# Optimization experiments

Measured on AMD Instinct MI355X. Metric: run time of the kernel, lower is better.

## Reference

```python
import jax, jax.numpy as jnp
import numpy as np

B, T, V = 4, 2048, 2048
D, H, L = 512, 8, 4
HD = D // H


def setup_inputs() -> dict:
    key = jax.random.key(0)
    ks = jax.random.split(key, 8)
    inp = {
        "x": jax.random.normal(ks[0], (B, T, V), dtype=jnp.float32),
        "token_embedding": jax.random.normal(ks[1], (D, V), dtype=jnp.float32),
        "position_embedding": jax.random.normal(ks[2], (T, D), dtype=jnp.float32),
        "Wk": jax.random.normal(ks[3], (L, D, D), dtype=jnp.float32),
        "Wq": jax.random.normal(ks[4], (L, D, D), dtype=jnp.float32),
        "Wv": jax.random.normal(ks[5], (L, D, D), dtype=jnp.float32),
        "Wp": jax.random.normal(ks[6], (L, D, D), dtype=jnp.float32),
        "readout": jax.random.normal(ks[7], (V, D), dtype=jnp.float32),
    }
    return inp


def _attention_block(h, wk, wq, wv, wp):
    # h: [B, T, D]; weights [D, D] (inner_dim == D since head_dim*num_heads == D)
    b, t, c = h.shape
    s = c ** (-0.5)

    def proj(w):
        # F.linear(h, w) = h @ w.T -> [B,T,D] -> [B,H,T,HD], scaled by C^{-1/2}
        return (jnp.einsum('btc,dc->btd', h, w) * s).reshape(b, t, H, HD).transpose(0, 2, 1, 3)

    q, k, v = proj(wq), proj(wk), proj(wv)
    scores = jnp.einsum('bhqd,bhkd->bhqk', q, k) * (HD ** (-0.5))  # [B,H,T,T]
    attn = jax.nn.softmax(scores, axis=-1)
    out = jnp.einsum('bhqk,bhkd->bhqd', attn, v)  # [B,H,T,HD]
    out = out.transpose(0, 2, 1, 3).reshape(b, t, c)
    # projection.size(-1) == inner_dim == D
    return jnp.einsum('btc,oc->bto', out, wp) * (c ** (-0.5))


def reference(x, token_embedding, position_embedding, Wk, Wq, Wv, Wp, readout):
    b, t, c = x.shape  # c == vocab_size
    tok = jnp.einsum('btv,dv->btd', x, token_embedding) * (c ** (-0.5))
    h = tok + position_embedding[:t]
    for l in range(L):
        h = _attention_block(h, Wk[l], Wq[l], Wv[l], Wp[l])
    # logits on last token; readout.size(-1) == D
    logits = jnp.einsum('bd,vd->bv', h[:, -1, :], readout) * (D ** (-0.5))
    return logits
```

## Files before the change

### kernel.cpp

```cpp
#include <hip/hip_runtime.h>
#include <math.h>

typedef __attribute__((ext_vector_type(4))) float    f32x4;
typedef __attribute__((ext_vector_type(2))) _Float16 f16x2;
typedef __attribute__((ext_vector_type(4))) _Float16 f16x4;
typedef __attribute__((ext_vector_type(8))) _Float16 f16x8;

constexpr int Bc  = 4;
constexpr int Tc  = 2048;
constexpr int Vc  = 2048;
constexpr int Dc  = 512;
constexpr int Hc  = 8;
constexpr int HDc = 64;
constexpr int Lc  = 4;
constexpr size_t SZe = (size_t)Bc * Tc * Dc;

constexpr float SM_C = 12.0f;

__device__ __forceinline__ void gload_lds16(const _Float16* g, _Float16* s) {
    __builtin_amdgcn_global_load_lds(
        (const __attribute__((address_space(1))) void*)g,
        (__attribute__((address_space(3))) void*)s,
        16, 0, 0);
}

__device__ __forceinline__ f16x2 cvt_pk(float a, float b) {
    return __builtin_bit_cast(f16x2, __builtin_amdgcn_cvt_pkrtz(a, b));
}

__global__ __launch_bounds__(256) void cvt_k(
    const float* __restrict__ in, _Float16* __restrict__ out, int n4)
{
    for (int i = blockIdx.x * 256 + threadIdx.x; i < n4; i += gridDim.x * 256) {
        float4 v = ((const float4*)in)[i];
        f16x4 h = {(_Float16)v.x, (_Float16)v.y, (_Float16)v.z, (_Float16)v.w};
        *(f16x4*)&out[(size_t)i * 4] = h;
    }
}

__global__ __launch_bounds__(256) void cvtW_k(
    const float* __restrict__ a, const float* __restrict__ b,
    const float* __restrict__ c, const float* __restrict__ d,
    _Float16* __restrict__ oa, _Float16* __restrict__ ob,
    _Float16* __restrict__ oc, _Float16* __restrict__ od, int n4)
{
    const float* in; _Float16* out;
    switch (blockIdx.y) {
        case 0:  in = a; out = oa; break;
        case 1:  in = b; out = ob; break;
        case 2:  in = c; out = oc; break;
        default: in = d; out = od; break;
    }
    for (int i = blockIdx.x * 256 + threadIdx.x; i < n4; i += gridDim.x * 256) {
        float4 v = ((const float4*)in)[i];
        f16x4 h = {(_Float16)v.x, (_Float16)v.y, (_Float16)v.z, (_Float16)v.w};
        *(f16x4*)&out[(size_t)i * 4] = h;
    }
}


template<bool QKV>
__global__ __launch_bounds__(256) void gemm_f16(
    const _Float16* __restrict__ A,
    const _Float16* __restrict__ W0, const _Float16* __restrict__ W1,
    const _Float16* __restrict__ W2,
    void* __restrict__ C0, const float* __restrict__ pos,
    int K, float scA, float scB)
{
    __shared__ __align__(16) _Float16 LA[2][128 * 64];
    __shared__ __align__(16) _Float16 LB[2][64 * 64];

    const int tid = threadIdx.x;
    const int w  = tid >> 6, l = tid & 63;
    const int li = l & 15,  lg = l >> 4;
    const int wm = w >> 1,  wn = w & 1;
    const int m0 = blockIdx.x * 128;

    int sec = 0, n0;
    const _Float16* Wb;
    if (QKV) {
        sec = blockIdx.y >> 3; n0 = (blockIdx.y & 7) * 64;
        Wb = (sec == 0) ? W0 : ((sec == 1) ? W1 : W2);
    } else {
        n0 = blockIdx.y * 64; Wb = W0;
    }
    const float scale = (sec == 0) ? scA : scB;

    const _Float16* srcA[4];
    const _Float16* srcB[2];
#pragma unroll
    for (int i = 0; i < 4; ++i) {
        const int d = i * 4096 + tid * 16;
        const int r = d >> 7, cb = (d & 127) ^ ((r & 7) << 4);
        srcA[i] = A + (size_t)(m0 + r) * K + (cb >> 1);
    }
#pragma unroll
    for (int i = 0; i < 2; ++i) {
        const int d = i * 4096 + tid * 16;
        const int r = d >> 7, cb = (d & 127) ^ ((r & 7) << 4);
        srcB[i] = Wb + (size_t)(n0 + r) * K + (cb >> 1);
    }

    auto stage = [&](int b) {
#pragma unroll
        for (int i = 0; i < 4; ++i) { gload_lds16(srcA[i], &LA[b][i * 2048 + tid * 8]); srcA[i] += 64; }
#pragma unroll
        for (int i = 0; i < 2; ++i) { gload_lds16(srcB[i], &LB[b][i * 2048 + tid * 8]); srcB[i] += 64; }
    };

    f32x4 acc[4][2];
#pragma unroll
    for (int i = 0; i < 4; ++i)
#pragma unroll
        for (int j = 0; j < 2; ++j) acc[i][j] = (f32x4){0.f, 0.f, 0.f, 0.f};

    auto compute = [&](int b) {
        const char* Ab = (const char*)&LA[b][0];
        const char* Bb = (const char*)&LB[b][0];
        f16x8 af[4][2], bf[2][2];
#pragma unroll
        for (int mb = 0; mb < 4; ++mb) {
            const int row = wm * 64 + mb * 16 + li, sz = (row & 7) << 4;
#pragma unroll
            for (int fi = 0; fi < 2; ++fi)
                af[mb][fi] = *(const f16x8*)(Ab + row * 128 + ((fi * 64 + lg * 16) ^ sz));
        }
#pragma unroll
        for (int nb = 0; nb < 2; ++nb) {
            const int row = wn * 32 + nb * 16 + li, sz = (row & 7) << 4;
#pragma unroll
            for (int fi = 0; fi < 2; ++fi)
                bf[nb][fi] = *(const f16x8*)(Bb + row * 128 + ((fi * 64 + lg * 16) ^ sz));
        }
#pragma unroll
        for (int mb = 0; mb < 4; ++mb)
#pragma unroll
            for (int nb = 0; nb < 2; ++nb)
#pragma unroll
                for (int fi = 0; fi < 2; ++fi)
                    acc[mb][nb] = __builtin_amdgcn_mfma_f32_16x16x32_f16(
                        af[mb][fi], bf[nb][fi], acc[mb][nb], 0, 0, 0);
    };

    const int NTk = K >> 6;
    stage(0);
    for (int kt = 0; kt < NTk; ++kt) {
        const int cur = kt & 1;
        if (kt + 1 < NTk) {
            stage(cur ^ 1);
            asm volatile("s_waitcnt vmcnt(6)" ::: "memory");
        } else {
            asm volatile("s_waitcnt vmcnt(0)" ::: "memory");
        }
        __builtin_amdgcn_s_barrier();
        __builtin_amdgcn_sched_barrier(0);
        compute(cur);
        __builtin_amdgcn_s_barrier();
        __builtin_amdgcn_sched_barrier(0);
    }

#pragma unroll
    for (int mb = 0; mb < 4; ++mb) {
#pragma unroll
        for (int nb = 0; nb < 2; ++nb) {
            const int mbase = m0 + wm * 64 + mb * 16 + lg * 4;
            const int nc    = n0 + wn * 32 + nb * 16 + li;
            if (QKV && sec == 2) {
                const int t = mbase & (Tc - 1);
                const int bh2 = (mbase >> 11) * Hc + (nc >> 6), d = nc & 63;
                f16x4 vv;
#pragma unroll
                for (int r = 0; r < 4; ++r) vv[r] = (_Float16)(acc[mb][nb][r] * scale);
                _Float16* vf = (_Float16*)C0 + 2 * SZe;
                const size_t adr =
                    (((size_t)bh2 * 32 + (t >> 6)) * 8 + ((d >> 4) & 3) * 2 + ((t >> 5) & 1)) * 512
                    + ((d & 15) + 16 * ((t >> 2) & 3)) * 8 + ((t >> 4) & 1) * 4;
                *(f16x4*)&vf[adr] = vv;
            } else if (QKV && sec == 1) {
                _Float16* kf = (_Float16*)C0 + SZe;
                const int t0 = mbase & (Tc - 1);
                const int bh2 = (mbase >> 11) * Hc + (nc >> 6), d = nc & 63;
                const size_t adr0 =
                    (((size_t)bh2 * 32 + (t0 >> 6)) * 8 + ((t0 >> 4) & 3) * 2 + (d >> 5)) * 512
                    + ((t0 & 15) + 16 * ((d >> 3) & 3)) * 8 + (d & 7);
#pragma unroll
                for (int r = 0; r < 4; ++r)
                    kf[adr0 + (size_t)r * 8] = (_Float16)(acc[mb][nb][r] * scale);
            } else if (QKV) {
                _Float16* outp = (_Float16*)C0;
#pragma unroll
                for (int r = 0; r < 4; ++r) {
                    const int m = mbase + r, bb2 = m >> 11, t = m & (Tc - 1);
                    outp[(((size_t)bb2 * Hc + (nc >> 6)) * Tc + t) * HDc + (nc & 63)] =
                        (_Float16)(acc[mb][nb][r] * scale);
                }
            } else {
                _Float16* outp = (_Float16*)C0;
#pragma unroll
                for (int r = 0; r < 4; ++r) {
                    const int m = mbase + r;
                    float val = acc[mb][nb][r] * scale;
                    if (pos) val += pos[(size_t)(m & (Tc - 1)) * Dc + nc];
                    outp[(size_t)m * Dc + nc] = (_Float16)val;
                }
            }
        }
    }
}

__global__ __launch_bounds__(256) void attn_mfma(
    const _Float16* __restrict__ Qh, const _Float16* __restrict__ Kf,
    const _Float16* __restrict__ Vf, _Float16* __restrict__ o)
{
    __shared__ __align__(16) _Float16 Ks[2][4096];
    __shared__ __align__(16) _Float16 Vs[2][4096];

    const int bid = blockIdx.x;
    const int bh  = bid & 31;
    const int qt  = bid >> 5;
    const int hh  = bh & (Hc - 1);
    const int bb  = bh >> 3;
    const int tid = threadIdx.x;
    const int w   = tid >> 6;
    const int l   = tid & 63;
    const int li  = l & 15, lg = l >> 4;
    const int q0  = qt * 64 + w * 16;

    const _Float16* Qb = Qh + (size_t)bh * Tc * HDc;

    f16x8 qf[2];
#pragma unroll
    for (int fi = 0; fi < 2; ++fi)
        qf[fi] = *(const f16x8*)&Qb[(size_t)(q0 + li) * HDc + fi * 32 + lg * 8];

    const _Float16* sK0 = Kf + (size_t)bh * Tc * HDc + tid * 8;
    const _Float16* sK1 = sK0 + 2048;
    const _Float16* sV0 = Vf + (size_t)bh * Tc * HDc + tid * 8;
    const _Float16* sV1 = sV0 + 2048;

    auto stage = [&](int b) {
        gload_lds16(sK0, &Ks[b][tid * 8]);
        gload_lds16(sK1, &Ks[b][2048 + tid * 8]);
        gload_lds16(sV0, &Vs[b][tid * 8]);
        gload_lds16(sV1, &Vs[b][2048 + tid * 8]);
        sK0 += 4096; sK1 += 4096; sV0 += 4096; sV1 += 4096;
    };

    f32x4 oacc[4];
#pragma unroll
    for (int dt = 0; dt < 4; ++dt) oacc[dt] = (f32x4){0.f, 0.f, 0.f, 0.f};
    f32x4 lacc = (f32x4){0.f, 0.f, 0.f, 0.f};
    const f16x4 ones = (f16x4){(_Float16)1.f, (_Float16)1.f, (_Float16)1.f, (_Float16)1.f};

    stage(0);
    constexpr int NT = Tc / 64;
    for (int kt = 0; kt < NT; ++kt) {
        const int cur = kt & 1;
        if (kt + 1 < NT) {
            stage(cur ^ 1);
            asm volatile("s_waitcnt vmcnt(4)" ::: "memory");
        } else {
            asm volatile("s_waitcnt vmcnt(0)" ::: "memory");
        }
        __builtin_amdgcn_s_barrier();
        __builtin_amdgcn_sched_barrier(0);

        const _Float16* KL = &Ks[cur][0];
        const _Float16* VL = &Vs[cur][0];

        f32x4 s[4];
        __builtin_amdgcn_s_setprio(1);
#pragma unroll
        for (int t = 0; t < 4; ++t) {
            s[t] = (f32x4){-SM_C, -SM_C, -SM_C, -SM_C};
#pragma unroll
            for (int fi = 0; fi < 2; ++fi) {
                f16x8 kfr = *(const f16x8*)(KL + (t * 2 + fi) * 512 + l * 8);
                s[t] = __builtin_amdgcn_mfma_f32_16x16x32_f16(kfr, qf[fi], s[t], 0, 0, 0);
            }
        }
        __builtin_amdgcn_s_setprio(0);

        f16x4 pf[4];
#pragma unroll
        for (int t = 0; t < 4; ++t) {
            float p0 = __builtin_amdgcn_exp2f(s[t][0]);
            float p1 = __builtin_amdgcn_exp2f(s[t][1]);
            float p2 = __builtin_amdgcn_exp2f(s[t][2]);
            float p3 = __builtin_amdgcn_exp2f(s[t][3]);
            f16x2 lo = cvt_pk(p0, p1);
            f16x2 hi = cvt_pk(p2, p3);
            pf[t] = (f16x4){lo[0], lo[1], hi[0], hi[1]};
        }

        __builtin_amdgcn_s_setprio(1);
#pragma unroll
        for (int t = 0; t < 4; ++t)
            lacc = __builtin_amdgcn_mfma_f32_16x16x16f16(ones, pf[t], lacc, 0, 0, 0);
#pragma unroll
        for (int dt = 0; dt < 4; ++dt) {
#pragma unroll
            for (int m = 0; m < 2; ++m) {
                f16x8 vv = *(const f16x8*)(VL + (dt * 2 + m) * 512 + l * 8);
                f16x4 vlo = (f16x4){vv[0], vv[1], vv[2], vv[3]};
                f16x4 vhi = (f16x4){vv[4], vv[5], vv[6], vv[7]};
                oacc[dt] = __builtin_amdgcn_mfma_f32_16x16x16f16(vlo, pf[2 * m],     oacc[dt], 0, 0, 0);
                oacc[dt] = __builtin_amdgcn_mfma_f32_16x16x16f16(vhi, pf[2 * m + 1], oacc[dt], 0, 0, 0);
            }
        }
        __builtin_amdgcn_s_setprio(0);

        __builtin_amdgcn_s_barrier();
        __builtin_amdgcn_sched_barrier(0);
    }

    const float inv = 1.f / lacc[0];
    _Float16* op = o + ((size_t)(bb * Tc + q0 + li) * Dc + hh * HDc + lg * 4);
#pragma unroll
    for (int dt = 0; dt < 4; ++dt) {
        f16x4 rv = {(_Float16)(oacc[dt][0] * inv), (_Float16)(oacc[dt][1] * inv),
                    (_Float16)(oacc[dt][2] * inv), (_Float16)(oacc[dt][3] * inv)};
        *(f16x4*)(op + dt * 16) = rv;
    }
}

__global__ __launch_bounds__(256) void readout_k(
    const _Float16* __restrict__ h, const float* __restrict__ ro,
    float* __restrict__ out, float scale)
{
    const int idx = blockIdx.x * 256 + threadIdx.x;
    const int vv  = idx & (Vc - 1);
    const int bb  = idx >> 11;
    const _Float16* hp = h + (size_t)(bb * Tc + (Tc - 1)) * Dc;
    const float* rp = ro + (size_t)vv * Dc;
    float ax = 0.f, ay = 0.f, az = 0.f, aw = 0.f;
#pragma unroll 8
    for (int i = 0; i < Dc / 4; ++i) {
        f16x4  hv = *(const f16x4*)(hp + i * 4);
        float4 rv = *(const float4*)(rp + i * 4);
        ax = fmaf((float)hv[0], rv.x, ax);
        ay = fmaf((float)hv[1], rv.y, ay);
        az = fmaf((float)hv[2], rv.z, az);
        aw = fmaf((float)hv[3], rv.w, aw);
    }
    out[idx] = ((ax + ay) + (az + aw)) * scale;
}

extern "C" void kernel_launch(void* const* d_in, const int* in_sizes, int n_in,
                              void* d_out, int out_size, void* d_ws, size_t ws_size,
                              hipStream_t stream)
{
    const float* x    = (const float*)d_in[0];
    const float* temb = (const float*)d_in[1];
    const float* pemb = (const float*)d_in[2];
    const float* Wk   = (const float*)d_in[3];
    const float* Wq   = (const float*)d_in[4];
    const float* Wv   = (const float*)d_in[5];
    const float* Wp   = (const float*)d_in[6];
    const float* ro   = (const float*)d_in[7];
    float* out = (float*)d_out;

    _Float16* h16    = (_Float16*)d_ws;
    _Float16* temb16 = h16 + SZe;
    _Float16* wq16   = temb16 + (size_t)Dc * Vc;
    _Float16* wk16   = wq16 + (size_t)Lc * Dc * Dc;
    _Float16* wv16   = wk16 + (size_t)Lc * Dc * Dc;
    _Float16* wp16   = wv16 + (size_t)Lc * Dc * Dc;
    _Float16* o16    = wp16 + (size_t)Lc * Dc * Dc;
    _Float16* qh     = o16 + SZe;
    _Float16* khF    = qh + SZe;
    _Float16* vhF    = khF + SZe;
    _Float16* x16    = o16;

    const float s_emb  = 1.0f / sqrtf((float)Vc);
    const float s_proj = 1.0f / sqrtf((float)Dc);
    const float s_q    = s_proj * 0.125f * 1.44269504f;

    const int W4 = Lc * Dc * Dc / 4;
    cvt_k<<<2048, 256, 0, stream>>>(x, x16, (int)SZe);
    cvt_k<<<512, 256, 0, stream>>>(temb, temb16, Dc * Vc / 4);
    cvtW_k<<<dim3(512, 4), 256, 0, stream>>>(Wq, Wk, Wv, Wp,
                                             wq16, wk16, wv16, wp16, W4);

    gemm_f16<false><<<dim3(64, 8), 256, 0, stream>>>(
        x16, temb16, nullptr, nullptr, h16, pemb, Vc, s_emb, s_emb);

    const size_t WOFF = (size_t)Dc * Dc;
    for (int lyr = 0; lyr < Lc; ++lyr) {
        gemm_f16<true><<<dim3(64, 24), 256, 0, stream>>>(
            h16, wq16 + lyr * WOFF, wk16 + lyr * WOFF, wv16 + lyr * WOFF,
            qh, nullptr, Dc, s_q, s_proj);

        attn_mfma<<<Bc * Hc * (Tc / 64), 256, 0, stream>>>(qh, khF, vhF, o16);

        gemm_f16<false><<<dim3(64, 8), 256, 0, stream>>>(
            o16, wp16 + lyr * WOFF, nullptr, nullptr, h16, nullptr, Dc, s_proj, s_proj);
    }

    readout_k<<<(Bc * Vc) / 256, 256, 0, stream>>>(h16, ro, out, s_proj);
}
```

Baseline: 409.9 us.

## Switch attention to 32x32x16 MFMA with two-wave blocks and permlane32 P transpose

```diff
diff --git a/kernel.cpp b/kernel.cpp
--- a/kernel.cpp
+++ b/kernel.cpp
@@ -1,10 +1,12 @@
 #include <hip/hip_runtime.h>
 #include <math.h>
 
-typedef __attribute__((ext_vector_type(4))) float    f32x4;
-typedef __attribute__((ext_vector_type(2))) _Float16 f16x2;
-typedef __attribute__((ext_vector_type(4))) _Float16 f16x4;
-typedef __attribute__((ext_vector_type(8))) _Float16 f16x8;
+typedef __attribute__((ext_vector_type(4)))  float    f32x4;
+typedef __attribute__((ext_vector_type(16))) float    f32x16;
+typedef __attribute__((ext_vector_type(2)))  _Float16 f16x2;
+typedef __attribute__((ext_vector_type(4)))  _Float16 f16x4;
+typedef __attribute__((ext_vector_type(8)))  _Float16 f16x8;
+typedef __attribute__((ext_vector_type(4)))  unsigned u32x4;
 
 constexpr int Bc  = 4;
 constexpr int Tc  = 2048;
@@ -24,8 +26,8 @@
         16, 0, 0);
 }
 
-__device__ __forceinline__ f16x2 cvt_pk(float a, float b) {
-    return __builtin_bit_cast(f16x2, __builtin_amdgcn_cvt_pkrtz(a, b));
+__device__ __forceinline__ unsigned cvt_pk_u(float a, float b) {
+    return __builtin_bit_cast(unsigned, __builtin_amdgcn_cvt_pkrtz(a, b));
 }
 
 __global__ __launch_bounds__(256) void cvt_k(
@@ -166,23 +168,23 @@
             const int mbase = m0 + wm * 64 + mb * 16 + lg * 4;
             const int nc    = n0 + wn * 32 + nb * 16 + li;
             if (QKV && sec == 2) {
-                const int t = mbase & (Tc - 1);
+                const int t0 = mbase & (Tc - 1);
                 const int bh2 = (mbase >> 11) * Hc + (nc >> 6), d = nc & 63;
                 f16x4 vv;
 #pragma unroll
                 for (int r = 0; r < 4; ++r) vv[r] = (_Float16)(acc[mb][nb][r] * scale);
                 _Float16* vf = (_Float16*)C0 + 2 * SZe;
                 const size_t adr =
-                    (((size_t)bh2 * 32 + (t >> 6)) * 8 + ((d >> 4) & 3) * 2 + ((t >> 5) & 1)) * 512
-                    + ((d & 15) + 16 * ((t >> 2) & 3)) * 8 + ((t >> 4) & 1) * 4;
+                    (((size_t)bh2 * 32 + (t0 >> 6)) * 8 + (d >> 5) * 4 + ((t0 >> 4) & 3)) * 512
+                    + ((d & 31) + 32 * ((t0 >> 3) & 1)) * 8 + (t0 & 7);
                 *(f16x4*)&vf[adr] = vv;
             } else if (QKV && sec == 1) {
                 _Float16* kf = (_Float16*)C0 + SZe;
                 const int t0 = mbase & (Tc - 1);
                 const int bh2 = (mbase >> 11) * Hc + (nc >> 6), d = nc & 63;
                 const size_t adr0 =
-                    (((size_t)bh2 * 32 + (t0 >> 6)) * 8 + ((t0 >> 4) & 3) * 2 + (d >> 5)) * 512
-                    + ((t0 & 15) + 16 * ((d >> 3) & 3)) * 8 + (d & 7);
+                    (((size_t)bh2 * 32 + (t0 >> 6)) * 8 + ((t0 >> 5) & 1) * 4 + (d >> 4)) * 512
+                    + ((t0 & 31) + 32 * ((d >> 3) & 1)) * 8 + (d & 7);
 #pragma unroll
                 for (int r = 0; r < 4; ++r)
                     kf[adr0 + (size_t)r * 8] = (_Float16)(acc[mb][nb][r] * scale);
@@ -208,7 +210,7 @@
     }
 }
 
-__global__ __launch_bounds__(256) void attn_mfma(
+__global__ __launch_bounds__(128) void attn_mfma(
     const _Float16* __restrict__ Qh, const _Float16* __restrict__ Kf,
     const _Float16* __restrict__ Vf, _Float16* __restrict__ o)
 {
@@ -223,34 +225,31 @@
     const int tid = threadIdx.x;
     const int w   = tid >> 6;
     const int l   = tid & 63;
-    const int li  = l & 15, lg = l >> 4;
-    const int q0  = qt * 64 + w * 16;
+    const int li  = l & 31, lg = l >> 5;
+    const int q0  = qt * 64 + w * 32;
 
     const _Float16* Qb = Qh + (size_t)bh * Tc * HDc;
-
-    f16x8 qf[2];
-#pragma unroll
-    for (int fi = 0; fi < 2; ++fi)
-        qf[fi] = *(const f16x8*)&Qb[(size_t)(q0 + li) * HDc + fi * 32 + lg * 8];
-
-    const _Float16* sK0 = Kf + (size_t)bh * Tc * HDc + tid * 8;
-    const _Float16* sK1 = sK0 + 2048;
-    const _Float16* sV0 = Vf + (size_t)bh * Tc * HDc + tid * 8;
-    const _Float16* sV1 = sV0 + 2048;
-
+    f16x8 qf[4];
+#pragma unroll
+    for (int fi = 0; fi < 4; ++fi)
+        qf[fi] = *(const f16x8*)&Qb[(size_t)(q0 + li) * HDc + fi * 16 + lg * 8];
+
+    const _Float16* sK = Kf + (size_t)bh * Tc * HDc + tid * 8;
+    const _Float16* sV = Vf + (size_t)bh * Tc * HDc + tid * 8;
     auto stage = [&](int b) {
-        gload_lds16(sK0, &Ks[b][tid * 8]);
-        gload_lds16(sK1, &Ks[b][2048 + tid * 8]);
-        gload_lds16(sV0, &Vs[b][tid * 8]);
-        gload_lds16(sV1, &Vs[b][2048 + tid * 8]);
-        sK0 += 4096; sK1 += 4096; sV0 += 4096; sV1 += 4096;
+#pragma unroll
+        for (int i = 0; i < 4; ++i) gload_lds16(sK + i * 1024, &Ks[b][i * 1024 + tid * 8]);
+#pragma unroll
+        for (int i = 0; i < 4; ++i) gload_lds16(sV + i * 1024, &Vs[b][i * 1024 + tid * 8]);
+        sK += 4096; sV += 4096;
     };
 
-    f32x4 oacc[4];
-#pragma unroll
-    for (int dt = 0; dt < 4; ++dt) oacc[dt] = (f32x4){0.f, 0.f, 0.f, 0.f};
-    f32x4 lacc = (f32x4){0.f, 0.f, 0.f, 0.f};
-    const f16x4 ones = (f16x4){(_Float16)1.f, (_Float16)1.f, (_Float16)1.f, (_Float16)1.f};
+    f32x16 oacc0, oacc1, lacc, sinit;
+#pragma unroll
+    for (int i = 0; i < 16; ++i) { oacc0[i] = 0.f; oacc1[i] = 0.f; lacc[i] = 0.f; sinit[i] = -SM_C; }
+    f16x8 ones;
+#pragma unroll
+    for (int i = 0; i < 8; ++i) ones[i] = (_Float16)1.f;
 
     stage(0);
     constexpr int NT = Tc / 64;
@@ -258,7 +257,7 @@
         const int cur = kt & 1;
         if (kt + 1 < NT) {
             stage(cur ^ 1);
-            asm volatile("s_waitcnt vmcnt(4)" ::: "memory");
+            asm volatile("s_waitcnt vmcnt(8)" ::: "memory");
         } else {
             asm volatile("s_waitcnt vmcnt(0)" ::: "memory");
         }
@@ -268,45 +267,52 @@
         const _Float16* KL = &Ks[cur][0];
         const _Float16* VL = &Vs[cur][0];
 
-        f32x4 s[4];
         __builtin_amdgcn_s_setprio(1);
-#pragma unroll
-        for (int t = 0; t < 4; ++t) {
-            s[t] = (f32x4){-SM_C, -SM_C, -SM_C, -SM_C};
-#pragma unroll
-            for (int fi = 0; fi < 2; ++fi) {
-                f16x8 kfr = *(const f16x8*)(KL + (t * 2 + fi) * 512 + l * 8);
-                s[t] = __builtin_amdgcn_mfma_f32_16x16x32_f16(kfr, qf[fi], s[t], 0, 0, 0);
-            }
+        f16x8 k00 = *(const f16x8*)(KL + 0 * 512 + l * 8);
+        f16x8 k10 = *(const f16x8*)(KL + 4 * 512 + l * 8);
+        f32x16 s0 = __builtin_amdgcn_mfma_f32_32x32x16_f16(k00, qf[0], sinit, 0, 0, 0);
+        f32x16 s1 = __builtin_amdgcn_mfma_f32_32x32x16_f16(k10, qf[0], sinit, 0, 0, 0);
+#pragma unroll
+        for (int fi = 1; fi < 4; ++fi) {
+            f16x8 ka = *(const f16x8*)(KL + (0 + fi) * 512 + l * 8);
+            f16x8 kb = *(const f16x8*)(KL + (4 + fi) * 512 + l * 8);
+            s0 = __builtin_amdgcn_mfma_f32_32x32x16_f16(ka, qf[fi], s0, 0, 0, 0);
+            s1 = __builtin_amdgcn_mfma_f32_32x32x16_f16(kb, qf[fi], s1, 0, 0, 0);
         }
         __builtin_amdgcn_s_setprio(0);
 
-        f16x4 pf[4];
-#pragma unroll
-        for (int t = 0; t < 4; ++t) {
-            float p0 = __builtin_amdgcn_exp2f(s[t][0]);
-            float p1 = __builtin_amdgcn_exp2f(s[t][1]);
-            float p2 = __builtin_amdgcn_exp2f(s[t][2]);
-            float p3 = __builtin_amdgcn_exp2f(s[t][3]);
-            f16x2 lo = cvt_pk(p0, p1);
-            f16x2 hi = cvt_pk(p2, p3);
-            pf[t] = (f16x4){lo[0], lo[1], hi[0], hi[1]};
+        unsigned cc[16];
+#pragma unroll
+        for (int g = 0; g < 4; ++g) {
+            cc[2 * g]     = cvt_pk_u(__builtin_amdgcn_exp2f(s0[4 * g + 0]),
+                                     __builtin_amdgcn_exp2f(s0[4 * g + 1]));
+            cc[2 * g + 1] = cvt_pk_u(__builtin_amdgcn_exp2f(s0[4 * g + 2]),
+                                     __builtin_amdgcn_exp2f(s0[4 * g + 3]));
+            cc[8 + 2 * g]     = cvt_pk_u(__builtin_amdgcn_exp2f(s1[4 * g + 0]),
+                                         __builtin_amdgcn_exp2f(s1[4 * g + 1]));
+            cc[8 + 2 * g + 1] = cvt_pk_u(__builtin_amdgcn_exp2f(s1[4 * g + 2]),
+                                         __builtin_amdgcn_exp2f(s1[4 * g + 3]));
+        }
+
+        f16x8 Bf[4];
+#pragma unroll
+        for (int ks = 0; ks < 4; ++ks) {
+            auto u = __builtin_amdgcn_permlane32_swap(cc[ks * 4 + 0], cc[ks * 4 + 2], false, false);
+            auto v = __builtin_amdgcn_permlane32_swap(cc[ks * 4 + 1], cc[ks * 4 + 3], false, false);
+            u32x4 b4 = (u32x4){u[0], v[0], u[1], v[1]};
+            Bf[ks] = __builtin_bit_cast(f16x8, b4);
         }
 
         __builtin_amdgcn_s_setprio(1);
 #pragma unroll
-        for (int t = 0; t < 4; ++t)
-            lacc = __builtin_amdgcn_mfma_f32_16x16x16f16(ones, pf[t], lacc, 0, 0, 0);
-#pragma unroll
-        for (int dt = 0; dt < 4; ++dt) {
-#pragma unroll
-            for (int m = 0; m < 2; ++m) {
-                f16x8 vv = *(const f16x8*)(VL + (dt * 2 + m) * 512 + l * 8);
-                f16x4 vlo = (f16x4){vv[0], vv[1], vv[2], vv[3]};
-                f16x4 vhi = (f16x4){vv[4], vv[5], vv[6], vv[7]};
-                oacc[dt] = __builtin_amdgcn_mfma_f32_16x16x16f16(vlo, pf[2 * m],     oacc[dt], 0, 0, 0);
-                oacc[dt] = __builtin_amdgcn_mfma_f32_16x16x16f16(vhi, pf[2 * m + 1], oacc[dt], 0, 0, 0);
-            }
+        for (int ks = 0; ks < 4; ++ks)
+            lacc = __builtin_amdgcn_mfma_f32_32x32x16_f16(ones, Bf[ks], lacc, 0, 0, 0);
+#pragma unroll
+        for (int ks = 0; ks < 4; ++ks) {
+            f16x8 v0 = *(const f16x8*)(VL + (0 + ks) * 512 + l * 8);
+            f16x8 v1 = *(const f16x8*)(VL + (4 + ks) * 512 + l * 8);
+            oacc0 = __builtin_amdgcn_mfma_f32_32x32x16_f16(v0, Bf[ks], oacc0, 0, 0, 0);
+            oacc1 = __builtin_amdgcn_mfma_f32_32x32x16_f16(v1, Bf[ks], oacc1, 0, 0, 0);
         }
         __builtin_amdgcn_s_setprio(0);
 
@@ -315,12 +321,16 @@
     }
 
     const float inv = 1.f / lacc[0];
-    _Float16* op = o + ((size_t)(bb * Tc + q0 + li) * Dc + hh * HDc + lg * 4);
-#pragma unroll
-    for (int dt = 0; dt < 4; ++dt) {
-        f16x4 rv = {(_Float16)(oacc[dt][0] * inv), (_Float16)(oacc[dt][1] * inv),
-                    (_Float16)(oacc[dt][2] * inv), (_Float16)(oacc[dt][3] * inv)};
-        *(f16x4*)(op + dt * 16) = rv;
+    _Float16* op = o + ((size_t)(bb * Tc + q0 + li) * Dc + hh * HDc);
+#pragma unroll
+    for (int g = 0; g < 4; ++g) {
+        const int d0 = 8 * g + 4 * lg;
+        f16x4 r0 = {(_Float16)(oacc0[4 * g + 0] * inv), (_Float16)(oacc0[4 * g + 1] * inv),
+                    (_Float16)(oacc0[4 * g + 2] * inv), (_Float16)(oacc0[4 * g + 3] * inv)};
+        f16x4 r1 = {(_Float16)(oacc1[4 * g + 0] * inv), (_Float16)(oacc1[4 * g + 1] * inv),
+                    (_Float16)(oacc1[4 * g + 2] * inv), (_Float16)(oacc1[4 * g + 3] * inv)};
+        *(f16x4*)(op + d0)      = r0;
+        *(f16x4*)(op + 32 + d0) = r1;
     }
 }
 
@@ -391,7 +401,7 @@
             h16, wq16 + lyr * WOFF, wk16 + lyr * WOFF, wv16 + lyr * WOFF,
             qh, nullptr, Dc, s_q, s_proj);
 
-        attn_mfma<<<Bc * Hc * (Tc / 64), 256, 0, stream>>>(qh, khF, vhF, o16);
+        attn_mfma<<<Bc * Hc * (Tc / 64), 128, 0, stream>>>(qh, khF, vhF, o16);
 
         gemm_f16<false><<<dim3(64, 8), 256, 0, stream>>>(
             o16, wp16 + lyr * WOFF, nullptr, nullptr, h16, nullptr, Dc, s_proj, s_proj);
```

Measured after the change: 434.5 us. 1.06x slower.
